# Optimization experiments

Measured on AMD Instinct MI355X. Metric: run time of the kernel, lower is better.

## Reference

```python
import jax, jax.numpy as jnp
import numpy as np

HEADS = 8
CHANNELS = 512
WINDOW = 129            # must be odd
W_HALF = (WINDOW - 1) // 2
B, S = 1, 2048


def setup_inputs() -> dict:
    key = jax.random.key(0)
    ks = jax.random.split(key, 7)
    C = CHANNELS
    x = jax.random.normal(ks[0], (B, C, S), dtype=jnp.float32)
    mask = jnp.ones((B, S), dtype=bool)
    scale = 1.0 / np.sqrt(C)
    Wq = jax.random.normal(ks[1], (C, C), dtype=jnp.float32) * scale
    bq = jax.random.normal(ks[2], (C,), dtype=jnp.float32) * 0.02
    Wk = jax.random.normal(ks[3], (C, C), dtype=jnp.float32) * scale
    bk = jax.random.normal(ks[4], (C,), dtype=jnp.float32) * 0.02
    Wv = jax.random.normal(ks[5], (C, C), dtype=jnp.float32) * scale
    bv = jax.random.normal(ks[6], (C,), dtype=jnp.float32) * 0.02
    return {"x": x, "mask": mask, "Wq": Wq, "bq": bq, "Wk": Wk, "bk": bk, "Wv": Wv, "bv": bv}


def reference(x, mask, Wq, bq, Wk, bk, Wv, bv):
    b, C, s = x.shape
    nh = HEADS
    h = C // nh
    xt = jnp.swapaxes(x, 1, 2)                      # [B, S, C]
    q = (xt @ Wq + bq).reshape(b, s, nh, h) * (h ** -0.5)
    k = (xt @ Wk + bk).reshape(b, s, nh, h)
    v = (xt @ Wv + bv).reshape(b, s, nh, h)
    # pad sequence dim by w on both sides (zeros, matching F.pad)
    kp = jnp.pad(k, ((0, 0), (W_HALF, W_HALF), (0, 0), (0, 0)))
    vp = jnp.pad(v, ((0, 0), (W_HALF, W_HALF), (0, 0), (0, 0)))
    pos = jnp.arange(s)[:, None] + jnp.arange(WINDOW)[None, :]  # [S, Wn]
    kw = kp[:, pos]                                  # [B, S, Wn, nh, h]
    vw = vp[:, pos]                                  # [B, S, Wn, nh, h]
    A = jnp.einsum('bqnh,bqjnh->bqjn', q, kw)        # [B, S, Wn, nh]
    mp = jnp.pad(mask, ((0, 0), (W_HALF, W_HALF)))   # pad with False
    mw = mp[:, pos]                                  # [B, S, Wn]
    neg = -jnp.finfo(A.dtype).max
    A = jnp.where(mw[..., None], A, neg)
    A = jax.nn.softmax(A, axis=2)                    # softmax over window dim
    z = jnp.einsum('bqjn,bqjnh->bqnh', A, vw)        # [B, S, nh, h]
    # faithful to original: transpose(1,2) then reshape(B, -1, nh*h)
    z = jnp.swapaxes(z, 1, 2).reshape(b, s, nh * h)
    return z
```

## Files before the change

### kernel.cpp

```cpp
#include <hip/hip_runtime.h>
#include <stdint.h>

#define SEQ 2048
#define CH  512
#define NHEAD 8
#define HDIM 64
#define VTS 2176

typedef __attribute__((ext_vector_type(8))) short bf16x8;
typedef __attribute__((ext_vector_type(8))) unsigned short u16x8;
typedef __attribute__((ext_vector_type(4))) float f32x4;

__device__ inline f32x4 mfma_bf16(bf16x8 a, bf16x8 b, f32x4 c) {
  return __builtin_amdgcn_mfma_f32_16x16x32_bf16(a, b, c, 0, 0, 0);
}

__device__ inline unsigned short f2bf(float f) {
  union { float f; unsigned int u; } v; v.f = f;
  unsigned int r = v.u + 0x7fffu + ((v.u >> 16) & 1u);
  return (unsigned short)(r >> 16);
}

__global__ __launch_bounds__(256) void prep_kernel(
    const float* __restrict__ x,
    const float* __restrict__ Wq, const float* __restrict__ Wk,
    const float* __restrict__ Wv,
    unsigned short* __restrict__ xt,
    unsigned short* __restrict__ wtq, unsigned short* __restrict__ wtk,
    unsigned short* __restrict__ wtv) {
  __shared__ float tile[64][65];
  int b = blockIdx.x;
  const float* in; unsigned short* out; int R, C, bx, by;
  if (b < 256)      { in = x;  out = xt;  R = 512; C = 2048; bx = b & 31;  by = b >> 5; }
  else if (b < 320) { in = Wq; out = wtq; R = 512; C = 512;  int t = b - 256; bx = t & 7; by = t >> 3; }
  else if (b < 384) { in = Wk; out = wtk; R = 512; C = 512;  int t = b - 320; bx = t & 7; by = t >> 3; }
  else              { in = Wv; out = wtv; R = 512; C = 512;  int t = b - 384; bx = t & 7; by = t >> 3; }
  int bc = bx * 64, br = by * 64;
  int tx = threadIdx.x & 63, tg = threadIdx.x >> 6;
  #pragma unroll
  for (int k = 0; k < 16; ++k) {
    int r = tg * 16 + k;
    tile[r][tx] = in[(br + r) * C + bc + tx];
  }
  __syncthreads();
  #pragma unroll
  for (int k = 0; k < 16; ++k) {
    int r = tg * 16 + k;
    out[(bc + r) * R + br + tx] = f2bf(tile[tx][r]);
  }
}

__global__ __launch_bounds__(256) void qkv_gemm(
    const unsigned short* __restrict__ A,
    const unsigned short* __restrict__ Bq, const unsigned short* __restrict__ Bk,
    const unsigned short* __restrict__ Bv,
    const float* __restrict__ bq, const float* __restrict__ bk,
    const float* __restrict__ bv,
    unsigned short* __restrict__ oq, unsigned short* __restrict__ ok,
    unsigned short* __restrict__ vt) {
  int z = blockIdx.z;
  const unsigned short* Bm = (z == 0) ? Bq : (z == 1) ? Bk : Bv;
  const float* bias = (z == 0) ? bq : (z == 1) ? bk : bv;
  float scale = (z == 0) ? 0.125f : 1.0f;

  int m0 = blockIdx.y * 64, n0 = blockIdx.x * 128;
  __shared__ unsigned short lA[64][40];
  __shared__ unsigned short lB[128][40];
  __shared__ unsigned short stg[4][16][40];
  int tid = threadIdx.x;
  int w = tid >> 6, l = tid & 63, l15 = l & 15, lq = l >> 4;
  int wr = w & 1, wc = w >> 1;

  if (z == 2 && blockIdx.y == 0) {
    #pragma unroll
    for (int i = 0; i < 32; ++i) {
      int q = i * 256 + tid;
      int r = q >> 6, c = q & 63;
      vt[(n0 + r) * VTS + c] = 0;
      vt[(n0 + r) * VTS + 64 + SEQ + c] = 0;
    }
  }

  f32x4 acc[2][4];
  #pragma unroll
  for (int m = 0; m < 2; ++m)
    #pragma unroll
    for (int n = 0; n < 4; ++n) acc[m][n] = (f32x4){0.f, 0.f, 0.f, 0.f};

  int srow = tid >> 2, scol = (tid & 3) * 8;
  for (int kk = 0; kk < 512; kk += 32) {
    *(u16x8*)&lA[srow][scol] = *(const u16x8*)&A[(m0 + srow) * 512 + kk + scol];
    #pragma unroll
    for (int it = 0; it < 2; ++it) {
      int row = it * 64 + srow;
      *(u16x8*)&lB[row][scol] = *(const u16x8*)&Bm[(n0 + row) * 512 + kk + scol];
    }
    __syncthreads();
    bf16x8 af[2], bfr[4];
    #pragma unroll
    for (int m = 0; m < 2; ++m) af[m]  = *(const bf16x8*)&lA[wr * 32 + m * 16 + l15][lq * 8];
    #pragma unroll
    for (int n = 0; n < 4; ++n) bfr[n] = *(const bf16x8*)&lB[wc * 64 + n * 16 + l15][lq * 8];
    #pragma unroll
    for (int m = 0; m < 2; ++m)
      #pragma unroll
      for (int n = 0; n < 4; ++n) acc[m][n] = mfma_bf16(af[m], bfr[n], acc[m][n]);
    __syncthreads();
  }

  if (z < 2) {
    unsigned short* outp = (z == 0) ? oq : ok;
    #pragma unroll
    for (int n = 0; n < 4; ++n) {
      int col = n0 + wc * 64 + n * 16 + l15;
      float b = bias[col];
      #pragma unroll
      for (int m = 0; m < 2; ++m) {
        int rowb = m0 + wr * 32 + m * 16 + lq * 4;
        #pragma unroll
        for (int r = 0; r < 4; ++r)
          outp[(rowb + r) * 512 + col] = f2bf((acc[m][n][r] + b) * scale);
      }
    }
  } else {
    int chan0 = n0 + wc * 64;
    int seq0  = m0 + wr * 32;
    #pragma unroll
    for (int nf = 0; nf < 4; ++nf) {
      float b = bias[chan0 + nf * 16 + l15];
      #pragma unroll
      for (int m = 0; m < 2; ++m)
        #pragma unroll
        for (int r = 0; r < 4; ++r)
          stg[w][l15][m * 16 + lq * 4 + r] = f2bf(acc[m][nf][r] + b);
      asm volatile("s_waitcnt lgkmcnt(0)" ::: "memory");
      #pragma unroll
      for (int i = 0; i < 8; ++i) {
        int r16 = 2 * i + (l >> 5);
        vt[(chan0 + nf * 16 + r16) * VTS + 64 + seq0 + (l & 31)] = stg[w][r16][l & 31];
      }
      asm volatile("s_waitcnt lgkmcnt(0)" ::: "memory");
    }
  }
}

__global__ __launch_bounds__(256) void attn_kernel(
    const unsigned short* __restrict__ qbf,
    const unsigned short* __restrict__ kbf,
    const unsigned short* __restrict__ vt,
    float* __restrict__ out) {
  int i0 = blockIdx.x * 64;
  int head = blockIdx.y;
  int w = threadIdx.x >> 6, l = threadIdx.x & 63;
  int l15 = l & 15, lq = l >> 4;
  int kbase = i0 - 64;

  __shared__ unsigned short pls[4][16][200];

  bf16x8 qa[2];
  {
    const unsigned short* qrow = qbf + (i0 + w * 16 + l15) * 512 + head * 64;
    qa[0] = *(const bf16x8*)(qrow + lq * 8);
    qa[1] = *(const bf16x8*)(qrow + 32 + lq * 8);
  }

  f32x4 sc[12];
  #pragma unroll
  for (int f = 0; f < 12; ++f) sc[f] = (f32x4){0.f, 0.f, 0.f, 0.f};
  #pragma unroll
  for (int f = 0; f < 12; ++f) {
    int kabs = kbase + f * 16 + l15;
    int kc = min(max(kabs, 0), SEQ - 1);
    const unsigned short* krow = kbf + kc * 512 + head * 64;
    bf16x8 b0 = *(const bf16x8*)(krow + lq * 8);
    bf16x8 b1 = *(const bf16x8*)(krow + 32 + lq * 8);
    sc[f] = mfma_bf16(qa[0], b0, sc[f]);
    sc[f] = mfma_bf16(qa[1], b1, sc[f]);
  }

  #pragma unroll
  for (int reg = 0; reg < 4; ++reg) {
    int ql = w * 16 + lq * 4 + reg;
    float m = -1e30f;
    #pragma unroll
    for (int f = 0; f < 12; ++f) {
      int c = f * 16 + l15;
      int kabs = kbase + c;
      bool valid = (c >= ql) && (c <= ql + 128) && (kabs >= 0) && (kabs < SEQ);
      float a = valid ? sc[f][reg] : -1e30f;
      sc[f][reg] = a;
      m = fmaxf(m, a);
    }
    #pragma unroll
    for (int d = 1; d < 16; d <<= 1) m = fmaxf(m, __shfl_xor(m, d));
    float s = 0.f;
    #pragma unroll
    for (int f = 0; f < 12; ++f) {
      float e = __expf(sc[f][reg] - m);
      s += e;
      sc[f][reg] = e;
    }
    #pragma unroll
    for (int d = 1; d < 16; d <<= 1) s += __shfl_xor(s, d);
    float inv = 1.0f / s;
    #pragma unroll
    for (int f = 0; f < 12; ++f) sc[f][reg] *= inv;
  }

  #pragma unroll
  for (int f = 0; f < 12; ++f)
    #pragma unroll
    for (int reg = 0; reg < 4; ++reg)
      pls[w][lq * 4 + reg][f * 16 + l15] = f2bf(sc[f][reg]);
  asm volatile("s_waitcnt lgkmcnt(0)" ::: "memory");

  f32x4 zacc[4];
  #pragma unroll
  for (int nf = 0; nf < 4; ++nf) zacc[nf] = (f32x4){0.f, 0.f, 0.f, 0.f};
  #pragma unroll
  for (int kf = 0; kf < 6; ++kf) {
    bf16x8 pa = *(const bf16x8*)&pls[w][l15][kf * 32 + lq * 8];
    #pragma unroll
    for (int nf = 0; nf < 4; ++nf) {
      const unsigned short* vrow =
          vt + (head * 64 + nf * 16 + l15) * VTS + 64 + kbase + kf * 32 + lq * 8;
      bf16x8 vb = *(const bf16x8*)vrow;
      zacc[nf] = mfma_bf16(pa, vb, zacc[nf]);
    }
  }

  #pragma unroll
  for (int nf = 0; nf < 4; ++nf)
    #pragma unroll
    for (int reg = 0; reg < 4; ++reg) {
      int q = i0 + w * 16 + lq * 4 + reg;
      int h = nf * 16 + l15;
      out[(head * 256 + (q >> 3)) * 512 + (q & 7) * 64 + h] = zacc[nf][reg];
    }
}

extern "C" void kernel_launch(void* const* d_in, const int* in_sizes, int n_in,
                              void* d_out, int out_size, void* d_ws, size_t ws_size,
                              hipStream_t stream) {
  const float* x  = (const float*)d_in[0];
  const float* Wq = (const float*)d_in[2];
  const float* bq = (const float*)d_in[3];
  const float* Wk = (const float*)d_in[4];
  const float* bk = (const float*)d_in[5];
  const float* Wv = (const float*)d_in[6];
  const float* bv = (const float*)d_in[7];
  float* out = (float*)d_out;

  char* base = (char*)d_ws;
  unsigned short* xt  = (unsigned short*)(base + 0);
  unsigned short* wtq = (unsigned short*)(base + 2097152);
  unsigned short* wtk = (unsigned short*)(base + 2621440);
  unsigned short* wtv = (unsigned short*)(base + 3145728);
  unsigned short* qbf = (unsigned short*)(base + 3670016);
  unsigned short* kbf = (unsigned short*)(base + 5767168);
  unsigned short* vt  = (unsigned short*)(base + 7864320);

  prep_kernel<<<448, 256, 0, stream>>>(x, Wq, Wk, Wv, xt, wtq, wtk, wtv);

  qkv_gemm<<<dim3(4, 32, 3), 256, 0, stream>>>(xt, wtq, wtk, wtv, bq, bk, bv,
                                               qbf, kbf, vt);

  attn_kernel<<<dim3(32, 8), 256, 0, stream>>>(qbf, kbf, vt, out);
}
```

Baseline: 97.04 us.

## Fuse fp32 transpose and bf16 conversion into QKV GEMM tile loads

Removes the separate prep kernel that transposed x and the weight matrices into bf16 workspace buffers. The GEMM now reads fp32 x and W directly, converts them to bf16 and writes them transposed into shared memory, using an XOR column swizzle so the scattered writes and the MFMA fragment reads avoid bank conflicts. This saves one kernel launch and a global write/read round trip of the bf16 copies. In exchange, each GEMM block redoes the fp32 loads and conversions for its tiles (x is re-read by every column block), and the per-element scalar LDS stores may be slower than the previous vector stores.

Measured after the change: 105.0 us. 1.08x slower.

```diff
diff --git a/kernel.cpp b/kernel.cpp
--- a/kernel.cpp
+++ b/kernel.cpp
@@ -8,7 +8,6 @@
 #define VTS 2176
 
 typedef __attribute__((ext_vector_type(8))) short bf16x8;
-typedef __attribute__((ext_vector_type(8))) unsigned short u16x8;
 typedef __attribute__((ext_vector_type(4))) float f32x4;
 
 __device__ inline f32x4 mfma_bf16(bf16x8 a, bf16x8 b, f32x4 c) {
@@ -21,45 +20,20 @@
   return (unsigned short)(r >> 16);
 }
 
-__global__ __launch_bounds__(256) void prep_kernel(
+__device__ inline int swizcol(int c, int r) {
+  return (((c >> 3) ^ ((r >> 3) & 3)) * 8) + (c & 7);
+}
+
+__global__ __launch_bounds__(256) void qkv_gemm(
     const float* __restrict__ x,
     const float* __restrict__ Wq, const float* __restrict__ Wk,
     const float* __restrict__ Wv,
-    unsigned short* __restrict__ xt,
-    unsigned short* __restrict__ wtq, unsigned short* __restrict__ wtk,
-    unsigned short* __restrict__ wtv) {
-  __shared__ float tile[64][65];
-  int b = blockIdx.x;
-  const float* in; unsigned short* out; int R, C, bx, by;
-  if (b < 256)      { in = x;  out = xt;  R = 512; C = 2048; bx = b & 31;  by = b >> 5; }
-  else if (b < 320) { in = Wq; out = wtq; R = 512; C = 512;  int t = b - 256; bx = t & 7; by = t >> 3; }
-  else if (b < 384) { in = Wk; out = wtk; R = 512; C = 512;  int t = b - 320; bx = t & 7; by = t >> 3; }
-  else              { in = Wv; out = wtv; R = 512; C = 512;  int t = b - 384; bx = t & 7; by = t >> 3; }
-  int bc = bx * 64, br = by * 64;
-  int tx = threadIdx.x & 63, tg = threadIdx.x >> 6;
-  #pragma unroll
-  for (int k = 0; k < 16; ++k) {
-    int r = tg * 16 + k;
-    tile[r][tx] = in[(br + r) * C + bc + tx];
-  }
-  __syncthreads();
-  #pragma unroll
-  for (int k = 0; k < 16; ++k) {
-    int r = tg * 16 + k;
-    out[(bc + r) * R + br + tx] = f2bf(tile[tx][r]);
-  }
-}
-
-__global__ __launch_bounds__(256) void qkv_gemm(
-    const unsigned short* __restrict__ A,
-    const unsigned short* __restrict__ Bq, const unsigned short* __restrict__ Bk,
-    const unsigned short* __restrict__ Bv,
     const float* __restrict__ bq, const float* __restrict__ bk,
     const float* __restrict__ bv,
     unsigned short* __restrict__ oq, unsigned short* __restrict__ ok,
     unsigned short* __restrict__ vt) {
   int z = blockIdx.z;
-  const unsigned short* Bm = (z == 0) ? Bq : (z == 1) ? Bk : Bv;
+  const float* Wm = (z == 0) ? Wq : (z == 1) ? Wk : Wv;
   const float* bias = (z == 0) ? bq : (z == 1) ? bk : bv;
   float scale = (z == 0) ? 0.125f : 1.0f;
 
@@ -87,20 +61,45 @@
     #pragma unroll
     for (int n = 0; n < 4; ++n) acc[m][n] = (f32x4){0.f, 0.f, 0.f, 0.f};
 
-  int srow = tid >> 2, scol = (tid & 3) * 8;
+  int c = tid >> 3, j = tid & 7;
   for (int kk = 0; kk < 512; kk += 32) {
-    *(u16x8*)&lA[srow][scol] = *(const u16x8*)&A[(m0 + srow) * 512 + kk + scol];
-    #pragma unroll
-    for (int it = 0; it < 2; ++it) {
-      int row = it * 64 + srow;
-      *(u16x8*)&lB[row][scol] = *(const u16x8*)&Bm[(n0 + row) * 512 + kk + scol];
+    {
+      const float* asrc = x + (size_t)(kk + c) * 2048 + m0 + j * 8;
+      float4 a0 = *(const float4*)asrc;
+      float4 a1 = *(const float4*)(asrc + 4);
+      float av[8] = {a0.x, a0.y, a0.z, a0.w, a1.x, a1.y, a1.z, a1.w};
+      #pragma unroll
+      for (int i = 0; i < 8; ++i) {
+        int r = j * 8 + i;
+        lA[r][swizcol(c, r)] = f2bf(av[i]);
+      }
+    }
+    {
+      const float* bsrc = Wm + (size_t)(kk + c) * 512 + n0 + j * 16;
+      float4 b0 = *(const float4*)bsrc;
+      float4 b1 = *(const float4*)(bsrc + 4);
+      float4 b2 = *(const float4*)(bsrc + 8);
+      float4 b3 = *(const float4*)(bsrc + 12);
+      float bvv[16] = {b0.x, b0.y, b0.z, b0.w, b1.x, b1.y, b1.z, b1.w,
+                       b2.x, b2.y, b2.z, b2.w, b3.x, b3.y, b3.z, b3.w};
+      #pragma unroll
+      for (int i = 0; i < 16; ++i) {
+        int r = j * 16 + i;
+        lB[r][swizcol(c, r)] = f2bf(bvv[i]);
+      }
     }
     __syncthreads();
     bf16x8 af[2], bfr[4];
     #pragma unroll
-    for (int m = 0; m < 2; ++m) af[m]  = *(const bf16x8*)&lA[wr * 32 + m * 16 + l15][lq * 8];
-    #pragma unroll
-    for (int n = 0; n < 4; ++n) bfr[n] = *(const bf16x8*)&lB[wc * 64 + n * 16 + l15][lq * 8];
+    for (int m = 0; m < 2; ++m) {
+      int row = wr * 32 + m * 16 + l15;
+      af[m] = *(const bf16x8*)&lA[row][(lq ^ ((row >> 3) & 3)) * 8];
+    }
+    #pragma unroll
+    for (int n = 0; n < 4; ++n) {
+      int row = wc * 64 + n * 16 + l15;
+      bfr[n] = *(const bf16x8*)&lB[row][(lq ^ ((row >> 3) & 3)) * 8];
+    }
     #pragma unroll
     for (int m = 0; m < 2; ++m)
       #pragma unroll
@@ -184,9 +183,9 @@
     float m = -1e30f;
     #pragma unroll
     for (int f = 0; f < 12; ++f) {
-      int c = f * 16 + l15;
-      int kabs = kbase + c;
-      bool valid = (c >= ql) && (c <= ql + 128) && (kabs >= 0) && (kabs < SEQ);
+      int cc = f * 16 + l15;
+      int kabs = kbase + cc;
+      bool valid = (cc >= ql) && (cc <= ql + 128) && (kabs >= 0) && (kabs < SEQ);
       float a = valid ? sc[f][reg] : -1e30f;
       sc[f][reg] = a;
       m = fmaxf(m, a);
@@ -252,17 +251,11 @@
   float* out = (float*)d_out;
 
   char* base = (char*)d_ws;
-  unsigned short* xt  = (unsigned short*)(base + 0);
-  unsigned short* wtq = (unsigned short*)(base + 2097152);
-  unsigned short* wtk = (unsigned short*)(base + 2621440);
-  unsigned short* wtv = (unsigned short*)(base + 3145728);
-  unsigned short* qbf = (unsigned short*)(base + 3670016);
-  unsigned short* kbf = (unsigned short*)(base + 5767168);
-  unsigned short* vt  = (unsigned short*)(base + 7864320);
-
-  prep_kernel<<<448, 256, 0, stream>>>(x, Wq, Wk, Wv, xt, wtq, wtk, wtv);
-
-  qkv_gemm<<<dim3(4, 32, 3), 256, 0, stream>>>(xt, wtq, wtk, wtv, bq, bk, bv,
+  unsigned short* qbf = (unsigned short*)(base + 0);
+  unsigned short* kbf = (unsigned short*)(base + 2097152);
+  unsigned short* vt  = (unsigned short*)(base + 4194304);
+
+  qkv_gemm<<<dim3(4, 32, 3), 256, 0, stream>>>(x, Wq, Wk, Wv, bq, bk, bv,
                                                qbf, kbf, vt);
 
   attn_kernel<<<dim3(32, 8), 256, 0, stream>>>(qbf, kbf, vt, out);
```

## Fuse Q, K, V projections into one GEMM block sharing the A tile

Applied to the files above, without the earlier changes.

The QKV GEMM now runs each block over all three weight matrices at once. Each 512-thread block loads the activation tile once and computes 64x64 tiles for Q, K and V, where before each projection was a separate grid slice that reloaded A. This cuts global A traffic and launches 256 larger blocks instead of 384. The cost is narrower 8-byte global loads, fewer MFMAs per wave per shared load, and a different occupancy profile.

New measurement: 98.19 us. No clear change (+1.2%).

```diff
diff --git a/kernel.cpp b/kernel.cpp
--- a/kernel.cpp
+++ b/kernel.cpp
@@ -50,7 +50,7 @@
   }
 }
 
-__global__ __launch_bounds__(256) void qkv_gemm(
+__global__ __launch_bounds__(512) void qkv_gemm3(
     const unsigned short* __restrict__ A,
     const unsigned short* __restrict__ Bq, const unsigned short* __restrict__ Bk,
     const unsigned short* __restrict__ Bv,
@@ -58,88 +58,78 @@
     const float* __restrict__ bv,
     unsigned short* __restrict__ oq, unsigned short* __restrict__ ok,
     unsigned short* __restrict__ vt) {
-  int z = blockIdx.z;
-  const unsigned short* Bm = (z == 0) ? Bq : (z == 1) ? Bk : Bv;
-  const float* bias = (z == 0) ? bq : (z == 1) ? bk : bv;
-  float scale = (z == 0) ? 0.125f : 1.0f;
-
-  int m0 = blockIdx.y * 64, n0 = blockIdx.x * 128;
+  int m0 = blockIdx.y * 64, n0 = blockIdx.x * 64;
   __shared__ unsigned short lA[64][40];
-  __shared__ unsigned short lB[128][40];
-  __shared__ unsigned short stg[4][16][40];
+  __shared__ unsigned short lB[3][64][40];
+  __shared__ unsigned short stg[8][16][40];
   int tid = threadIdx.x;
   int w = tid >> 6, l = tid & 63, l15 = l & 15, lq = l >> 4;
-  int wr = w & 1, wc = w >> 1;
-
-  if (z == 2 && blockIdx.y == 0) {
-    #pragma unroll
-    for (int i = 0; i < 32; ++i) {
-      int q = i * 256 + tid;
+  int wr = w >> 2, wc = w & 3;
+
+  if (blockIdx.y == 0) {
+    #pragma unroll
+    for (int i = 0; i < 8; ++i) {
+      int q = i * 512 + tid;
       int r = q >> 6, c = q & 63;
       vt[(n0 + r) * VTS + c] = 0;
       vt[(n0 + r) * VTS + 64 + SEQ + c] = 0;
     }
   }
 
-  f32x4 acc[2][4];
-  #pragma unroll
-  for (int m = 0; m < 2; ++m)
-    #pragma unroll
-    for (int n = 0; n < 4; ++n) acc[m][n] = (f32x4){0.f, 0.f, 0.f, 0.f};
-
-  int srow = tid >> 2, scol = (tid & 3) * 8;
+  f32x4 acc[3][2];
+  #pragma unroll
+  for (int z = 0; z < 3; ++z)
+    #pragma unroll
+    for (int m = 0; m < 2; ++m) acc[z][m] = (f32x4){0.f, 0.f, 0.f, 0.f};
+
+  int srow = tid >> 3, scol = (tid & 7) * 4;
   for (int kk = 0; kk < 512; kk += 32) {
-    *(u16x8*)&lA[srow][scol] = *(const u16x8*)&A[(m0 + srow) * 512 + kk + scol];
-    #pragma unroll
-    for (int it = 0; it < 2; ++it) {
-      int row = it * 64 + srow;
-      *(u16x8*)&lB[row][scol] = *(const u16x8*)&Bm[(n0 + row) * 512 + kk + scol];
-    }
+    *(uint2*)&lA[srow][scol]    = *(const uint2*)&A[(m0 + srow) * 512 + kk + scol];
+    *(uint2*)&lB[0][srow][scol] = *(const uint2*)&Bq[(n0 + srow) * 512 + kk + scol];
+    *(uint2*)&lB[1][srow][scol] = *(const uint2*)&Bk[(n0 + srow) * 512 + kk + scol];
+    *(uint2*)&lB[2][srow][scol] = *(const uint2*)&Bv[(n0 + srow) * 512 + kk + scol];
     __syncthreads();
-    bf16x8 af[2], bfr[4];
-    #pragma unroll
-    for (int m = 0; m < 2; ++m) af[m]  = *(const bf16x8*)&lA[wr * 32 + m * 16 + l15][lq * 8];
-    #pragma unroll
-    for (int n = 0; n < 4; ++n) bfr[n] = *(const bf16x8*)&lB[wc * 64 + n * 16 + l15][lq * 8];
+    bf16x8 af[2], bfr[3];
+    #pragma unroll
+    for (int m = 0; m < 2; ++m) af[m] = *(const bf16x8*)&lA[wr * 32 + m * 16 + l15][lq * 8];
+    #pragma unroll
+    for (int z = 0; z < 3; ++z) bfr[z] = *(const bf16x8*)&lB[z][wc * 16 + l15][lq * 8];
+    #pragma unroll
+    for (int z = 0; z < 3; ++z)
+      #pragma unroll
+      for (int m = 0; m < 2; ++m) acc[z][m] = mfma_bf16(af[m], bfr[z], acc[z][m]);
+    __syncthreads();
+  }
+
+  #pragma unroll
+  for (int z = 0; z < 2; ++z) {
+    unsigned short* outp = (z == 0) ? oq : ok;
+    const float* bias = (z == 0) ? bq : bk;
+    float scale = (z == 0) ? 0.125f : 1.0f;
+    int col = n0 + wc * 16 + l15;
+    float b = bias[col];
+    #pragma unroll
+    for (int m = 0; m < 2; ++m) {
+      int rowb = m0 + wr * 32 + m * 16 + lq * 4;
+      #pragma unroll
+      for (int r = 0; r < 4; ++r)
+        outp[(rowb + r) * 512 + col] = f2bf((acc[z][m][r] + b) * scale);
+    }
+  }
+  {
+    int chan0 = n0 + wc * 16;
+    int seq0  = m0 + wr * 32;
+    float b = bv[chan0 + l15];
     #pragma unroll
     for (int m = 0; m < 2; ++m)
       #pragma unroll
-      for (int n = 0; n < 4; ++n) acc[m][n] = mfma_bf16(af[m], bfr[n], acc[m][n]);
-    __syncthreads();
-  }
-
-  if (z < 2) {
-    unsigned short* outp = (z == 0) ? oq : ok;
-    #pragma unroll
-    for (int n = 0; n < 4; ++n) {
-      int col = n0 + wc * 64 + n * 16 + l15;
-      float b = bias[col];
-      #pragma unroll
-      for (int m = 0; m < 2; ++m) {
-        int rowb = m0 + wr * 32 + m * 16 + lq * 4;
-        #pragma unroll
-        for (int r = 0; r < 4; ++r)
-          outp[(rowb + r) * 512 + col] = f2bf((acc[m][n][r] + b) * scale);
-      }
-    }
-  } else {
-    int chan0 = n0 + wc * 64;
-    int seq0  = m0 + wr * 32;
-    #pragma unroll
-    for (int nf = 0; nf < 4; ++nf) {
-      float b = bias[chan0 + nf * 16 + l15];
-      #pragma unroll
-      for (int m = 0; m < 2; ++m)
-        #pragma unroll
-        for (int r = 0; r < 4; ++r)
-          stg[w][l15][m * 16 + lq * 4 + r] = f2bf(acc[m][nf][r] + b);
-      asm volatile("s_waitcnt lgkmcnt(0)" ::: "memory");
-      #pragma unroll
-      for (int i = 0; i < 8; ++i) {
-        int r16 = 2 * i + (l >> 5);
-        vt[(chan0 + nf * 16 + r16) * VTS + 64 + seq0 + (l & 31)] = stg[w][r16][l & 31];
-      }
-      asm volatile("s_waitcnt lgkmcnt(0)" ::: "memory");
+      for (int r = 0; r < 4; ++r)
+        stg[w][l15][m * 16 + lq * 4 + r] = f2bf(acc[2][m][r] + b);
+    asm volatile("s_waitcnt lgkmcnt(0)" ::: "memory");
+    #pragma unroll
+    for (int i = 0; i < 8; ++i) {
+      int r16 = 2 * i + (l >> 5);
+      vt[(chan0 + r16) * VTS + 64 + seq0 + (l & 31)] = stg[w][r16][l & 31];
     }
   }
 }
@@ -184,9 +174,9 @@
     float m = -1e30f;
     #pragma unroll
     for (int f = 0; f < 12; ++f) {
-      int c = f * 16 + l15;
-      int kabs = kbase + c;
-      bool valid = (c >= ql) && (c <= ql + 128) && (kabs >= 0) && (kabs < SEQ);
+      int cc = f * 16 + l15;
+      int kabs = kbase + cc;
+      bool valid = (cc >= ql) && (cc <= ql + 128) && (kabs >= 0) && (kabs < SEQ);
       float a = valid ? sc[f][reg] : -1e30f;
       sc[f][reg] = a;
       m = fmaxf(m, a);
@@ -262,8 +252,8 @@
 
   prep_kernel<<<448, 256, 0, stream>>>(x, Wq, Wk, Wv, xt, wtq, wtk, wtv);
 
-  qkv_gemm<<<dim3(4, 32, 3), 256, 0, stream>>>(xt, wtq, wtk, wtv, bq, bk, bv,
-                                               qbf, kbf, vt);
+  qkv_gemm3<<<dim3(8, 32), 512, 0, stream>>>(xt, wtq, wtk, wtv, bq, bk, bv,
+                                             qbf, kbf, vt);
 
   attn_kernel<<<dim3(32, 8), 256, 0, stream>>>(qbf, kbf, vt, out);
 }
```

## Register-prefetch QKV GEMM tiles with K=64 steps over concatenated weights

Applied to the files above, without the earlier changes.

The QKV GEMM now walks K in steps of 64 instead of 32, halving the number of barrier pairs. It prefetches the next tile from global memory into registers while MFMAs run on the current LDS tile. The three weight matrices are addressed as one concatenated buffer through a 12x32 grid, on the assumption that wtq, wtk and wtv sit contiguously in the workspace. The cost is more LDS per block and more registers, which may reduce occupancy.

Measured after the change: 95.94 us. Within noise of the previous version (-1.1%).

```diff
diff --git a/kernel.cpp b/kernel.cpp
--- a/kernel.cpp
+++ b/kernel.cpp
@@ -50,34 +50,31 @@
   }
 }
 
-__global__ __launch_bounds__(256) void qkv_gemm(
+__global__ __launch_bounds__(256) void gemm_qkv(
     const unsigned short* __restrict__ A,
-    const unsigned short* __restrict__ Bq, const unsigned short* __restrict__ Bk,
-    const unsigned short* __restrict__ Bv,
+    const unsigned short* __restrict__ Bc,
     const float* __restrict__ bq, const float* __restrict__ bk,
     const float* __restrict__ bv,
     unsigned short* __restrict__ oq, unsigned short* __restrict__ ok,
     unsigned short* __restrict__ vt) {
-  int z = blockIdx.z;
-  const unsigned short* Bm = (z == 0) ? Bq : (z == 1) ? Bk : Bv;
-  const float* bias = (z == 0) ? bq : (z == 1) ? bk : bv;
-  float scale = (z == 0) ? 0.125f : 1.0f;
-
-  int m0 = blockIdx.y * 64, n0 = blockIdx.x * 128;
-  __shared__ unsigned short lA[64][40];
-  __shared__ unsigned short lB[128][40];
+  int n0 = blockIdx.x * 128;
+  int m0 = blockIdx.y * 64;
+  int z = n0 >> 9;
+  __shared__ unsigned short lA[64][72];
+  __shared__ unsigned short lB[128][72];
   __shared__ unsigned short stg[4][16][40];
   int tid = threadIdx.x;
   int w = tid >> 6, l = tid & 63, l15 = l & 15, lq = l >> 4;
   int wr = w & 1, wc = w >> 1;
 
   if (z == 2 && blockIdx.y == 0) {
+    int cn0 = n0 - 1024;
     #pragma unroll
     for (int i = 0; i < 32; ++i) {
       int q = i * 256 + tid;
       int r = q >> 6, c = q & 63;
-      vt[(n0 + r) * VTS + c] = 0;
-      vt[(n0 + r) * VTS + 64 + SEQ + c] = 0;
+      vt[(cn0 + r) * VTS + c] = 0;
+      vt[(cn0 + r) * VTS + 64 + SEQ + c] = 0;
     }
   }
 
@@ -87,32 +84,53 @@
     #pragma unroll
     for (int n = 0; n < 4; ++n) acc[m][n] = (f32x4){0.f, 0.f, 0.f, 0.f};
 
-  int srow = tid >> 2, scol = (tid & 3) * 8;
-  for (int kk = 0; kk < 512; kk += 32) {
-    *(u16x8*)&lA[srow][scol] = *(const u16x8*)&A[(m0 + srow) * 512 + kk + scol];
-    #pragma unroll
-    for (int it = 0; it < 2; ++it) {
-      int row = it * 64 + srow;
-      *(u16x8*)&lB[row][scol] = *(const u16x8*)&Bm[(n0 + row) * 512 + kk + scol];
-    }
+  int srow = tid >> 2, scol = (tid & 3) * 16;
+  const unsigned short* apr = &A[(m0 + srow) * 512 + scol];
+  const unsigned short* bpr0 = &Bc[(n0 + srow) * 512 + scol];
+  const unsigned short* bpr1 = &Bc[(n0 + 64 + srow) * 512 + scol];
+
+  u16x8 a0 = *(const u16x8*)apr,        a1 = *(const u16x8*)(apr + 8);
+  u16x8 b0 = *(const u16x8*)bpr0,       b1 = *(const u16x8*)(bpr0 + 8);
+  u16x8 b2 = *(const u16x8*)bpr1,       b3 = *(const u16x8*)(bpr1 + 8);
+
+  for (int t = 0; t < 8; ++t) {
+    *(u16x8*)&lA[srow][scol]          = a0;
+    *(u16x8*)&lA[srow][scol + 8]      = a1;
+    *(u16x8*)&lB[srow][scol]          = b0;
+    *(u16x8*)&lB[srow][scol + 8]      = b1;
+    *(u16x8*)&lB[64 + srow][scol]     = b2;
+    *(u16x8*)&lB[64 + srow][scol + 8] = b3;
     __syncthreads();
-    bf16x8 af[2], bfr[4];
-    #pragma unroll
-    for (int m = 0; m < 2; ++m) af[m]  = *(const bf16x8*)&lA[wr * 32 + m * 16 + l15][lq * 8];
-    #pragma unroll
-    for (int n = 0; n < 4; ++n) bfr[n] = *(const bf16x8*)&lB[wc * 64 + n * 16 + l15][lq * 8];
-    #pragma unroll
-    for (int m = 0; m < 2; ++m)
-      #pragma unroll
-      for (int n = 0; n < 4; ++n) acc[m][n] = mfma_bf16(af[m], bfr[n], acc[m][n]);
+    if (t < 7) {
+      int kk = (t + 1) * 64;
+      a0 = *(const u16x8*)(apr + kk);   a1 = *(const u16x8*)(apr + kk + 8);
+      b0 = *(const u16x8*)(bpr0 + kk);  b1 = *(const u16x8*)(bpr0 + kk + 8);
+      b2 = *(const u16x8*)(bpr1 + kk);  b3 = *(const u16x8*)(bpr1 + kk + 8);
+    }
+    #pragma unroll
+    for (int ks = 0; ks < 2; ++ks) {
+      bf16x8 af[2], bfr[4];
+      #pragma unroll
+      for (int m = 0; m < 2; ++m)
+        af[m] = *(const bf16x8*)&lA[wr * 32 + m * 16 + l15][ks * 32 + lq * 8];
+      #pragma unroll
+      for (int n = 0; n < 4; ++n)
+        bfr[n] = *(const bf16x8*)&lB[wc * 64 + n * 16 + l15][ks * 32 + lq * 8];
+      #pragma unroll
+      for (int m = 0; m < 2; ++m)
+        #pragma unroll
+        for (int n = 0; n < 4; ++n) acc[m][n] = mfma_bf16(af[m], bfr[n], acc[m][n]);
+    }
     __syncthreads();
   }
 
   if (z < 2) {
     unsigned short* outp = (z == 0) ? oq : ok;
+    const float* bias = (z == 0) ? bq : bk;
+    float scale = (z == 0) ? 0.125f : 1.0f;
     #pragma unroll
     for (int n = 0; n < 4; ++n) {
-      int col = n0 + wc * 64 + n * 16 + l15;
+      int col = (n0 & 511) + wc * 64 + n * 16 + l15;
       float b = bias[col];
       #pragma unroll
       for (int m = 0; m < 2; ++m) {
@@ -123,11 +141,11 @@
       }
     }
   } else {
-    int chan0 = n0 + wc * 64;
+    int chan0 = (n0 - 1024) + wc * 64;
     int seq0  = m0 + wr * 32;
     #pragma unroll
     for (int nf = 0; nf < 4; ++nf) {
-      float b = bias[chan0 + nf * 16 + l15];
+      float b = bv[chan0 + nf * 16 + l15];
       #pragma unroll
       for (int m = 0; m < 2; ++m)
         #pragma unroll
@@ -184,9 +202,9 @@
     float m = -1e30f;
     #pragma unroll
     for (int f = 0; f < 12; ++f) {
-      int c = f * 16 + l15;
-      int kabs = kbase + c;
-      bool valid = (c >= ql) && (c <= ql + 128) && (kabs >= 0) && (kabs < SEQ);
+      int cc = f * 16 + l15;
+      int kabs = kbase + cc;
+      bool valid = (cc >= ql) && (cc <= ql + 128) && (kabs >= 0) && (kabs < SEQ);
       float a = valid ? sc[f][reg] : -1e30f;
       sc[f][reg] = a;
       m = fmaxf(m, a);
@@ -262,8 +280,7 @@
 
   prep_kernel<<<448, 256, 0, stream>>>(x, Wq, Wk, Wv, xt, wtq, wtk, wtv);
 
-  qkv_gemm<<<dim3(4, 32, 3), 256, 0, stream>>>(xt, wtq, wtk, wtv, bq, bk, bv,
-                                               qbf, kbf, vt);
+  gemm_qkv<<<dim3(12, 32), 256, 0, stream>>>(xt, wtq, bq, bk, bv, qbf, kbf, vt);
 
   attn_kernel<<<dim3(32, 8), 256, 0, stream>>>(qbf, kbf, vt, out);
 }
```
